# Kernel optimization log

Hardware: AMD Instinct MI355X
Metric: run time of the kernel (lower is better)

The kernel has to match this reference:

```python
import jax, jax.numpy as jnp
import numpy as np

D = 768          # n_embd
I = 3072         # moe_intermediate_size (4 * n_embd)
E = 8            # n_routed_experts
K = 2            # num_experts_per_tok
LIMIT = 10.0     # swiglu_limit
VOCAB = 32768


def setup_inputs() -> dict:
    key = jax.random.key(0)
    ks = jax.random.split(key, 10)
    s = 0.02
    return {
        "x": jax.random.normal(ks[0], (1, 2048, D), dtype=jnp.float32),
        "input_ids": jax.random.randint(ks[1], (1, 2048), 0, VOCAB, dtype=jnp.int64),
        "gate_w": jax.random.normal(ks[2], (D, E), dtype=jnp.float32) * s,
        "gate_bias": jnp.zeros((E,), dtype=jnp.float32),
        "w1": jax.random.normal(ks[3], (E, D, I), dtype=jnp.float32) * s,
        "w2": jax.random.normal(ks[4], (E, I, D), dtype=jnp.float32) * s,
        "w3": jax.random.normal(ks[5], (E, D, I), dtype=jnp.float32) * s,
        "w1s": jax.random.normal(ks[6], (D, I), dtype=jnp.float32) * s,
        "w2s": jax.random.normal(ks[7], (I, D), dtype=jnp.float32) * s,
        "w3s": jax.random.normal(ks[8], (D, I), dtype=jnp.float32) * s,
    }


def _expert(xf, W1, W2, W3):
    # SwiGLU with asymmetric clamping, as in DeepSeekExpert (swiglu_limit > 0)
    gate = jnp.minimum(xf @ W1, LIMIT)               # clamp max only
    up = jnp.clip(xf @ W3, -LIMIT, LIMIT)            # clamp both sides
    return (jax.nn.silu(gate) * up) @ W2


def reference(x, input_ids, gate_w, gate_bias, w1, w2, w3, w1s, w2s, w3s):
    B, T, _ = x.shape
    flat = x.reshape(-1, D)                           # [N, D], N = B*T
    N = flat.shape[0]

    # gating: sqrtsoftplus scoring
    scores = jnp.sqrt(jax.nn.softplus(flat @ gate_w))  # [N, E]
    routed_scores = scores + gate_bias                 # gate_bias used only for topk selection
    _, indices = jax.lax.top_k(routed_scores, K)       # [N, K]

    weights = jnp.take_along_axis(scores, indices, axis=1)  # [N, K]
    # norm_topk_prob=True; routed_scaling_factor=1.0
    weights = weights / jnp.clip(weights.sum(axis=-1, keepdims=True), 1e-6)

    # dense combine matrix [N, E] (jit-friendly dispatch/combine)
    combine = jnp.zeros((N, E), dtype=weights.dtype)
    combine = combine.at[jnp.arange(N)[:, None], indices].add(weights)

    # shared expert on all tokens
    y = _expert(flat, w1s, w2s, w3s)                   # [N, D]

    # routed experts: batched grouped GEMM over all tokens, then weighted combine
    gate_h = jnp.minimum(jnp.einsum('td,edi->eti', flat, w1), LIMIT)   # [E, N, I]
    up_h = jnp.clip(jnp.einsum('td,edi->eti', flat, w3), -LIMIT, LIMIT)
    h = jax.nn.silu(gate_h) * up_h                     # [E, N, I]
    out_e = jnp.einsum('eti,eid->etd', h, w2)          # [E, N, D]
    routed = jnp.einsum('etd,te->td', out_e, combine)  # [N, D]

    return (y + routed).reshape(B, T, D)
```

## Files before the change

kernel.cpp:

```cpp
#include <hip/hip_runtime.h>


#define D_ 768
#define I_ 3072
#define E_ 8
#define NTOK 2048
#define NPMAX 5120
#define MAXTILES 40
#define NSHT 16

typedef __bf16 bf16x8 __attribute__((ext_vector_type(8)));
typedef float floatx4 __attribute__((ext_vector_type(4)));

__device__ __forceinline__ unsigned short f2b(float f) {
    unsigned int u = __float_as_uint(f);
    u += 0x7fffu + ((u >> 16) & 1u);
    return (unsigned short)(u >> 16);
}


__global__ void tcast_kernel(const float* __restrict__ src,
                             unsigned short* __restrict__ dst, int R, int C) {
    __shared__ float t[32][33];
    const float* s = src + (size_t)blockIdx.z * R * C;
    unsigned short* d = dst + (size_t)blockIdx.z * R * C;
    int c0 = blockIdx.x * 32, r0 = blockIdx.y * 32;
    int tx = threadIdx.x & 31, ty = threadIdx.x >> 5;
#pragma unroll
    for (int j = 0; j < 4; j++) {
        int r = ty + j * 8;
        t[r][tx] = s[(size_t)(r0 + r) * C + c0 + tx];
    }
    __syncthreads();
#pragma unroll
    for (int j = 0; j < 4; j++) {
        int c = ty + j * 8;
        d[(size_t)(c0 + c) * R + r0 + tx] = f2b(t[tx][c]);
    }
}

__global__ void cast_x_kernel(const float* __restrict__ x,
                              unsigned short* __restrict__ xb) {
    int gid = blockIdx.x * 256 + threadIdx.x;
    float4 v = *(const float4*)(x + (size_t)gid * 4);
    ushort4 o;
    o.x = f2b(v.x); o.y = f2b(v.y); o.z = f2b(v.z); o.w = f2b(v.w);
    *(ushort4*)(xb + (size_t)gid * 4) = o;
}


__global__ void gate_topk_kernel(const float* __restrict__ x,
                                 const float* __restrict__ gw,
                                 const float* __restrict__ gb,
                                 int* __restrict__ idx, float* __restrict__ wts) {
    int t = blockIdx.x * 4 + (threadIdx.x >> 6);
    int lane = threadIdx.x & 63;
    float z[E_];
#pragma unroll
    for (int e = 0; e < E_; e++) z[e] = 0.f;
    const float* xr = x + (size_t)t * D_;
    for (int j = lane; j < D_; j += 64) {
        float xv = xr[j];
        const float* g = gw + (size_t)j * E_;
#pragma unroll
        for (int e = 0; e < E_; e++) z[e] += xv * g[e];
    }
#pragma unroll
    for (int off = 32; off > 0; off >>= 1)
#pragma unroll
        for (int e = 0; e < E_; e++) z[e] += __shfl_down(z[e], off, 64);
    if (lane == 0) {
        float s[E_], r[E_];
#pragma unroll
        for (int e = 0; e < E_; e++) {
            float zz = z[e];
            float sp = zz > 0.f ? zz + log1pf(expf(-zz)) : log1pf(expf(zz));
            s[e] = sqrtf(sp);
            r[e] = s[e] + gb[e];
        }
        int i0 = 0;
        for (int e = 1; e < E_; e++) if (r[e] > r[i0]) i0 = e;
        int i1 = (i0 == 0) ? 1 : 0;
        for (int e = 0; e < E_; e++) if (e != i0 && r[e] > r[i1]) i1 = e;
        float w0 = s[i0], w1 = s[i1];
        float inv = 1.f / fmaxf(w0 + w1, 1e-6f);
        idx[2 * t] = i0; idx[2 * t + 1] = i1;
        wts[2 * t] = w0 * inv; wts[2 * t + 1] = w1 * inv;
    }
}


__global__ void route_build_kernel(const int* __restrict__ idx,
                                   const float* __restrict__ wts,
                                   int* __restrict__ pair_token,
                                   float* __restrict__ pair_w,
                                   int* __restrict__ pos_of,
                                   int* __restrict__ tiles) {
    __shared__ int cnt[E_], seg[E_], cur[E_];
    int tid = threadIdx.x;
    if (tid < E_) { cnt[tid] = 0; cur[tid] = 0; }
    __syncthreads();
    for (int p = tid; p < NTOK * 2; p += 256) atomicAdd(&cnt[idx[p]], 1);
    __syncthreads();
    if (tid == 0) {
        int off = 0, nt = 0;
        for (int e = 0; e < E_; e++) {
            seg[e] = off;
            int te = (cnt[e] + 127) >> 7;
            for (int j = 0; j < te; j++) {
                tiles[nt * 2] = e; tiles[nt * 2 + 1] = off + j * 128; nt++;
            }
            off += te * 128;
        }
        for (; nt < MAXTILES; nt++) { tiles[nt * 2] = -1; tiles[nt * 2 + 1] = 0; }
    }
    for (int p = tid; p < NPMAX; p += 256) pair_token[p] = -1;
    __syncthreads();
    for (int p = tid; p < NTOK * 2; p += 256) {
        int e = idx[p];
        int r = atomicAdd(&cur[e], 1);
        int pos = seg[e] + r;
        pair_token[pos] = p >> 1;
        pair_w[pos] = wts[p];
        pos_of[p] = pos;
    }
}

__global__ void gather_kernel(const unsigned short* __restrict__ xb,
                              const int* __restrict__ pair_token,
                              unsigned short* __restrict__ xg) {
    int gid = blockIdx.x * 256 + threadIdx.x;
    int p = gid / (D_ / 8);
    int j = (gid % (D_ / 8)) * 8;
    int t = pair_token[p];
    int4 v = make_int4(0, 0, 0, 0);
    if (t >= 0) v = *(const int4*)(xb + (size_t)t * D_ + j);
    *(int4*)(xg + (size_t)p * D_ + j) = v;
}


__launch_bounds__(256)
__global__ void gemm_act_kernel(const unsigned short* __restrict__ xb,
                                const unsigned short* __restrict__ xg,
                                const unsigned short* __restrict__ w1sb,
                                const unsigned short* __restrict__ w3sb,
                                const unsigned short* __restrict__ w1b,
                                const unsigned short* __restrict__ w3b,
                                const int* __restrict__ tiles,
                                unsigned short* __restrict__ act_s,
                                unsigned short* __restrict__ act_r) {
    __shared__ __align__(16) unsigned short As[128 * 40];
    __shared__ __align__(16) unsigned short Bs1[64 * 40];
    __shared__ __align__(16) unsigned short Bs3[64 * 40];

    int mt = blockIdx.y;
    const unsigned short *A, *B1, *B3;
    unsigned short* C;
    int m0;
    if (mt < NSHT) {
        A = xb; B1 = w1sb; B3 = w3sb; C = act_s; m0 = mt * 128;
    } else {
        int e = tiles[(mt - NSHT) * 2];
        if (e < 0) return;
        m0 = tiles[(mt - NSHT) * 2 + 1];
        A = xg; B1 = w1b + (size_t)e * I_ * D_; B3 = w3b + (size_t)e * I_ * D_;
        C = act_r;
    }
    int n0 = blockIdx.x * 64;
    int tid = threadIdx.x;
    int lane = tid & 63, wave = tid >> 6;
    int wm = (wave & 1) * 64, wn = (wave >> 1) * 32;
    int l15 = lane & 15, quad = lane >> 4;

    int arow0 = tid >> 2, cc0 = (tid & 3) * 8;
    int arow1 = arow0 + 64;
    int brow = tid >> 2;

    floatx4 acc1[4][2] = {}; floatx4 acc3[4][2] = {};

    for (int k0 = 0; k0 < D_; k0 += 32) {
        __syncthreads();
        int4 va0 = *(const int4*)(A + (size_t)(m0 + arow0) * D_ + k0 + cc0);
        int4 va1 = *(const int4*)(A + (size_t)(m0 + arow1) * D_ + k0 + cc0);
        int4 vb1 = *(const int4*)(B1 + (size_t)(n0 + brow) * D_ + k0 + cc0);
        int4 vb3 = *(const int4*)(B3 + (size_t)(n0 + brow) * D_ + k0 + cc0);
        *(int4*)(As + arow0 * 40 + cc0) = va0;
        *(int4*)(As + arow1 * 40 + cc0) = va1;
        *(int4*)(Bs1 + brow * 40 + cc0) = vb1;
        *(int4*)(Bs3 + brow * 40 + cc0) = vb3;
        __syncthreads();

        bf16x8 af[4], b1f[2], b3f[2];
#pragma unroll
        for (int mi = 0; mi < 4; mi++)
            af[mi] = *(const bf16x8*)(As + (wm + mi * 16 + l15) * 40 + quad * 8);
#pragma unroll
        for (int ni = 0; ni < 2; ni++) {
            b1f[ni] = *(const bf16x8*)(Bs1 + (wn + ni * 16 + l15) * 40 + quad * 8);
            b3f[ni] = *(const bf16x8*)(Bs3 + (wn + ni * 16 + l15) * 40 + quad * 8);
        }
#pragma unroll
        for (int mi = 0; mi < 4; mi++)
#pragma unroll
            for (int ni = 0; ni < 2; ni++) {
                acc1[mi][ni] = __builtin_amdgcn_mfma_f32_16x16x32_bf16(
                    af[mi], b1f[ni], acc1[mi][ni], 0, 0, 0);
                acc3[mi][ni] = __builtin_amdgcn_mfma_f32_16x16x32_bf16(
                    af[mi], b3f[ni], acc3[mi][ni], 0, 0, 0);
            }
    }

#pragma unroll
    for (int mi = 0; mi < 4; mi++)
#pragma unroll
        for (int ni = 0; ni < 2; ni++) {
            int col = n0 + wn + ni * 16 + l15;
#pragma unroll
            for (int r = 0; r < 4; r++) {
                int row = m0 + wm + mi * 16 + quad * 4 + r;
                float g = fminf(acc1[mi][ni][r], 10.f);
                float u = fminf(fmaxf(acc3[mi][ni][r], -10.f), 10.f);
                float a = g / (1.f + __expf(-g)) * u;
                C[(size_t)row * I_ + col] = f2b(a);
            }
        }
}


__launch_bounds__(256)
__global__ void gemm_out_kernel(const unsigned short* __restrict__ act_s,
                                const unsigned short* __restrict__ act_r,
                                const unsigned short* __restrict__ w2sb,
                                const unsigned short* __restrict__ w2b,
                                const int* __restrict__ tiles,
                                float* __restrict__ y_s, float* __restrict__ ro) {
    __shared__ __align__(16) unsigned short As[128 * 40];
    __shared__ __align__(16) unsigned short Bs[64 * 40];

    int mt = blockIdx.y;
    const unsigned short *A, *B;
    float* C;
    int m0;
    if (mt < NSHT) {
        A = act_s; B = w2sb; C = y_s; m0 = mt * 128;
    } else {
        int e = tiles[(mt - NSHT) * 2];
        if (e < 0) return;
        m0 = tiles[(mt - NSHT) * 2 + 1];
        A = act_r; B = w2b + (size_t)e * I_ * D_; C = ro;
    }
    int n0 = blockIdx.x * 64;
    int tid = threadIdx.x;
    int lane = tid & 63, wave = tid >> 6;
    int wm = (wave & 1) * 64, wn = (wave >> 1) * 32;
    int l15 = lane & 15, quad = lane >> 4;

    int arow0 = tid >> 2, cc0 = (tid & 3) * 8;
    int arow1 = arow0 + 64;
    int brow = tid >> 2;

    floatx4 acc[4][2] = {};

    for (int k0 = 0; k0 < I_; k0 += 32) {
        __syncthreads();
        int4 va0 = *(const int4*)(A + (size_t)(m0 + arow0) * I_ + k0 + cc0);
        int4 va1 = *(const int4*)(A + (size_t)(m0 + arow1) * I_ + k0 + cc0);
        int4 vb  = *(const int4*)(B + (size_t)(n0 + brow) * I_ + k0 + cc0);
        *(int4*)(As + arow0 * 40 + cc0) = va0;
        *(int4*)(As + arow1 * 40 + cc0) = va1;
        *(int4*)(Bs + brow * 40 + cc0) = vb;
        __syncthreads();

        bf16x8 af[4], bf[2];
#pragma unroll
        for (int mi = 0; mi < 4; mi++)
            af[mi] = *(const bf16x8*)(As + (wm + mi * 16 + l15) * 40 + quad * 8);
#pragma unroll
        for (int ni = 0; ni < 2; ni++)
            bf[ni] = *(const bf16x8*)(Bs + (wn + ni * 16 + l15) * 40 + quad * 8);
#pragma unroll
        for (int mi = 0; mi < 4; mi++)
#pragma unroll
            for (int ni = 0; ni < 2; ni++)
                acc[mi][ni] = __builtin_amdgcn_mfma_f32_16x16x32_bf16(
                    af[mi], bf[ni], acc[mi][ni], 0, 0, 0);
    }

#pragma unroll
    for (int mi = 0; mi < 4; mi++)
#pragma unroll
        for (int ni = 0; ni < 2; ni++) {
            int col = n0 + wn + ni * 16 + l15;
#pragma unroll
            for (int r = 0; r < 4; r++) {
                int row = m0 + wm + mi * 16 + quad * 4 + r;
                C[(size_t)row * D_ + col] = acc[mi][ni][r];
            }
        }
}


__global__ void combine_kernel(const float* __restrict__ y_s,
                               const float* __restrict__ ro,
                               const int* __restrict__ pos_of,
                               const float* __restrict__ pair_w,
                               float* __restrict__ out) {
    int gid = blockIdx.x * 256 + threadIdx.x;
    int t = gid / (D_ / 4);
    int j = (gid % (D_ / 4)) * 4;
    int p0 = pos_of[2 * t], p1 = pos_of[2 * t + 1];
    float w0 = pair_w[p0], w1 = pair_w[p1];
    float4 a = *(const float4*)(y_s + (size_t)t * D_ + j);
    float4 b = *(const float4*)(ro + (size_t)p0 * D_ + j);
    float4 c = *(const float4*)(ro + (size_t)p1 * D_ + j);
    float4 o;
    o.x = a.x + w0 * b.x + w1 * c.x;
    o.y = a.y + w0 * b.y + w1 * c.y;
    o.z = a.z + w0 * b.z + w1 * c.z;
    o.w = a.w + w0 * b.w + w1 * c.w;
    *(float4*)(out + (size_t)t * D_ + j) = o;
}


extern "C" void kernel_launch(void* const* d_in, const int* in_sizes, int n_in,
                              void* d_out, int out_size, void* d_ws, size_t ws_size,
                              hipStream_t stream) {
    (void)in_sizes; (void)n_in; (void)out_size; (void)ws_size;
    const float* x   = (const float*)d_in[0];
    const float* gw  = (const float*)d_in[2];
    const float* gb  = (const float*)d_in[3];
    const float* w1  = (const float*)d_in[4];
    const float* w2  = (const float*)d_in[5];
    const float* w3  = (const float*)d_in[6];
    const float* w1s = (const float*)d_in[7];
    const float* w2s = (const float*)d_in[8];
    const float* w3s = (const float*)d_in[9];
    float* out = (float*)d_out;

    char* ws = (char*)d_ws;
    size_t off = 0;
    auto alloc = [&](size_t bytes) {
        size_t o = (off + 255) & ~(size_t)255;
        off = o + bytes;
        return (void*)(ws + o);
    };
    unsigned short* xb   = (unsigned short*)alloc((size_t)NTOK * D_ * 2);
    unsigned short* xg   = (unsigned short*)alloc((size_t)NPMAX * D_ * 2);
    unsigned short* w1b  = (unsigned short*)alloc((size_t)E_ * I_ * D_ * 2);
    unsigned short* w3b  = (unsigned short*)alloc((size_t)E_ * I_ * D_ * 2);
    unsigned short* w2b  = (unsigned short*)alloc((size_t)E_ * I_ * D_ * 2);
    unsigned short* w1sb = (unsigned short*)alloc((size_t)I_ * D_ * 2);
    unsigned short* w3sb = (unsigned short*)alloc((size_t)I_ * D_ * 2);
    unsigned short* w2sb = (unsigned short*)alloc((size_t)I_ * D_ * 2);
    unsigned short* acts = (unsigned short*)alloc((size_t)NTOK * I_ * 2);
    unsigned short* actr = (unsigned short*)alloc((size_t)NPMAX * I_ * 2);
    float* ys   = (float*)alloc((size_t)NTOK * D_ * 4);
    float* rout = (float*)alloc((size_t)NPMAX * D_ * 4);
    int*   idx  = (int*)alloc((size_t)NTOK * 2 * 4);
    float* wts  = (float*)alloc((size_t)NTOK * 2 * 4);
    int*   ptok = (int*)alloc((size_t)NPMAX * 4);
    float* pw   = (float*)alloc((size_t)NPMAX * 4);
    int*   posf = (int*)alloc((size_t)NTOK * 2 * 4);
    int*   tls  = (int*)alloc((size_t)MAXTILES * 2 * 4);

    tcast_kernel<<<dim3(I_ / 32, D_ / 32, E_), 256, 0, stream>>>(w1, w1b, D_, I_);
    tcast_kernel<<<dim3(I_ / 32, D_ / 32, E_), 256, 0, stream>>>(w3, w3b, D_, I_);
    tcast_kernel<<<dim3(D_ / 32, I_ / 32, E_), 256, 0, stream>>>(w2, w2b, I_, D_);
    tcast_kernel<<<dim3(I_ / 32, D_ / 32, 1), 256, 0, stream>>>(w1s, w1sb, D_, I_);
    tcast_kernel<<<dim3(I_ / 32, D_ / 32, 1), 256, 0, stream>>>(w3s, w3sb, D_, I_);
    tcast_kernel<<<dim3(D_ / 32, I_ / 32, 1), 256, 0, stream>>>(w2s, w2sb, I_, D_);

    cast_x_kernel<<<NTOK * D_ / 4 / 256, 256, 0, stream>>>(x, xb);
    gate_topk_kernel<<<NTOK / 4, 256, 0, stream>>>(x, gw, gb, idx, wts);
    route_build_kernel<<<1, 256, 0, stream>>>(idx, wts, ptok, pw, posf, tls);
    gather_kernel<<<NPMAX * (D_ / 8) / 256, 256, 0, stream>>>(xb, ptok, xg);

    gemm_act_kernel<<<dim3(I_ / 64, NSHT + MAXTILES), 256, 0, stream>>>(
        xb, xg, w1sb, w3sb, w1b, w3b, tls, acts, actr);
    gemm_out_kernel<<<dim3(D_ / 64, NSHT + MAXTILES), 256, 0, stream>>>(
        acts, actr, w2sb, w2b, tls, ys, rout);
    combine_kernel<<<NTOK * (D_ / 4) / 256, 256, 0, stream>>>(ys, rout, posf, pw, out);
}
```

Baseline: 519.4 us.

## Use direct global-to-LDS loads in GEMMs and fuse wider weight transpose-cast kernels

Replaces the register-staged global→LDS tile copies in both GEMM kernels with global_load_lds 16-byte direct loads, dropping the LDS row padding (stride 40→32) so each wave writes a contiguous 16-row slab. The six weight transpose/cast launches become two launches with 64x64 tiles, float4 reads and 16-byte bf16 writes. The aim is fewer VGPR round-trips and instructions on the load path and less launch overhead and narrower memory traffic in the weight casting. Removing the padding may introduce LDS bank conflicts on the fragment reads.

Result: faster. 474.1 us (-8.7%).

```diff
diff --git a/kernel.cpp b/kernel.cpp
--- a/kernel.cpp
+++ b/kernel.cpp
@@ -12,6 +12,10 @@
 typedef __bf16 bf16x8 __attribute__((ext_vector_type(8)));
 typedef float floatx4 __attribute__((ext_vector_type(4)));
 
+#define GLOAD_LDS16(g, l) __builtin_amdgcn_global_load_lds( \
+    (const __attribute__((address_space(1))) void*)(g),     \
+    (__attribute__((address_space(3))) void*)(l), 16, 0, 0)
+
 __device__ __forceinline__ unsigned short f2b(float f) {
     unsigned int u = __float_as_uint(f);
     u += 0x7fffu + ((u >> 16) & 1u);
@@ -19,24 +23,61 @@
 }
 
 
-__global__ void tcast_kernel(const float* __restrict__ src,
-                             unsigned short* __restrict__ dst, int R, int C) {
-    __shared__ float t[32][33];
-    const float* s = src + (size_t)blockIdx.z * R * C;
-    unsigned short* d = dst + (size_t)blockIdx.z * R * C;
-    int c0 = blockIdx.x * 32, r0 = blockIdx.y * 32;
-    int tx = threadIdx.x & 31, ty = threadIdx.x >> 5;
+template <int R, int C>
+__device__ __forceinline__ void tbody(const float* __restrict__ s,
+                                      unsigned short* __restrict__ d) {
+    __shared__ float t[64][65];
+    int c0 = blockIdx.x * 64, r0 = blockIdx.y * 64;
+    int tid = threadIdx.x;
 #pragma unroll
     for (int j = 0; j < 4; j++) {
-        int r = ty + j * 8;
-        t[r][tx] = s[(size_t)(r0 + r) * C + c0 + tx];
+        int slot = tid + j * 256;
+        int r = slot >> 4;
+        int c4 = (slot & 15) * 4;
+        float4 v = *(const float4*)(s + (size_t)(r0 + r) * C + c0 + c4);
+        t[r][c4] = v.x; t[r][c4 + 1] = v.y; t[r][c4 + 2] = v.z; t[r][c4 + 3] = v.w;
     }
     __syncthreads();
 #pragma unroll
-    for (int j = 0; j < 4; j++) {
-        int c = ty + j * 8;
-        d[(size_t)(c0 + c) * R + r0 + tx] = f2b(t[tx][c]);
-    }
+    for (int j = 0; j < 2; j++) {
+        int slot = tid + j * 256;
+        int c = slot >> 3;
+        int rs = (slot & 7) * 8;
+        unsigned short o[8];
+#pragma unroll
+        for (int i = 0; i < 8; i++) o[i] = f2b(t[rs + i][c]);
+        *(int4*)(d + (size_t)(c0 + c) * R + r0 + rs) = *(const int4*)o;
+    }
+}
+
+__global__ void tcastDI_kernel(const float* __restrict__ w1,
+                               const float* __restrict__ w3,
+                               const float* __restrict__ w1s,
+                               const float* __restrict__ w3s,
+                               unsigned short* __restrict__ w1b,
+                               unsigned short* __restrict__ w3b,
+                               unsigned short* __restrict__ w1sb,
+                               unsigned short* __restrict__ w3sb) {
+    int z = blockIdx.z;
+    const float* s;
+    unsigned short* d;
+    if (z < 8)        { s = w1 + (size_t)z * D_ * I_;       d = w1b + (size_t)z * D_ * I_; }
+    else if (z < 16)  { s = w3 + (size_t)(z - 8) * D_ * I_; d = w3b + (size_t)(z - 8) * D_ * I_; }
+    else if (z == 16) { s = w1s; d = w1sb; }
+    else              { s = w3s; d = w3sb; }
+    tbody<D_, I_>(s, d);
+}
+
+__global__ void tcastID_kernel(const float* __restrict__ w2,
+                               const float* __restrict__ w2s,
+                               unsigned short* __restrict__ w2b,
+                               unsigned short* __restrict__ w2sb) {
+    int z = blockIdx.z;
+    const float* s;
+    unsigned short* d;
+    if (z < 8) { s = w2 + (size_t)z * I_ * D_; d = w2b + (size_t)z * I_ * D_; }
+    else       { s = w2s; d = w2sb; }
+    tbody<I_, D_>(s, d);
 }
 
 __global__ void cast_x_kernel(const float* __restrict__ x,
@@ -149,9 +190,9 @@
                                 const int* __restrict__ tiles,
                                 unsigned short* __restrict__ act_s,
                                 unsigned short* __restrict__ act_r) {
-    __shared__ __align__(16) unsigned short As[128 * 40];
-    __shared__ __align__(16) unsigned short Bs1[64 * 40];
-    __shared__ __align__(16) unsigned short Bs3[64 * 40];
+    __shared__ __align__(16) unsigned short As[128 * 32];
+    __shared__ __align__(16) unsigned short Bs1[64 * 32];
+    __shared__ __align__(16) unsigned short Bs3[64 * 32];
 
     int mt = blockIdx.y;
     const unsigned short *A, *B1, *B3;
@@ -171,33 +212,35 @@
     int lane = tid & 63, wave = tid >> 6;
     int wm = (wave & 1) * 64, wn = (wave >> 1) * 32;
     int l15 = lane & 15, quad = lane >> 4;
-
-    int arow0 = tid >> 2, cc0 = (tid & 3) * 8;
-    int arow1 = arow0 + 64;
-    int brow = tid >> 2;
+    int l4 = lane >> 2, c8 = (lane & 3) * 8;
+
+    const unsigned short* Ap0 = A + (size_t)(m0 + wave * 16 + l4) * D_ + c8;
+    const unsigned short* Ap1 = Ap0 + (size_t)64 * D_;
+    const unsigned short* B1p = B1 + (size_t)(n0 + wave * 16 + l4) * D_ + c8;
+    const unsigned short* B3p = B3 + (size_t)(n0 + wave * 16 + l4) * D_ + c8;
+    unsigned short* AsW0 = As + wave * 16 * 32;
+    unsigned short* AsW1 = As + (64 + wave * 16) * 32;
+    unsigned short* Bs1W = Bs1 + wave * 16 * 32;
+    unsigned short* Bs3W = Bs3 + wave * 16 * 32;
 
     floatx4 acc1[4][2] = {}; floatx4 acc3[4][2] = {};
 
     for (int k0 = 0; k0 < D_; k0 += 32) {
         __syncthreads();
-        int4 va0 = *(const int4*)(A + (size_t)(m0 + arow0) * D_ + k0 + cc0);
-        int4 va1 = *(const int4*)(A + (size_t)(m0 + arow1) * D_ + k0 + cc0);
-        int4 vb1 = *(const int4*)(B1 + (size_t)(n0 + brow) * D_ + k0 + cc0);
-        int4 vb3 = *(const int4*)(B3 + (size_t)(n0 + brow) * D_ + k0 + cc0);
-        *(int4*)(As + arow0 * 40 + cc0) = va0;
-        *(int4*)(As + arow1 * 40 + cc0) = va1;
-        *(int4*)(Bs1 + brow * 40 + cc0) = vb1;
-        *(int4*)(Bs3 + brow * 40 + cc0) = vb3;
+        GLOAD_LDS16(Ap0 + k0, AsW0);
+        GLOAD_LDS16(Ap1 + k0, AsW1);
+        GLOAD_LDS16(B1p + k0, Bs1W);
+        GLOAD_LDS16(B3p + k0, Bs3W);
         __syncthreads();
 
         bf16x8 af[4], b1f[2], b3f[2];
 #pragma unroll
         for (int mi = 0; mi < 4; mi++)
-            af[mi] = *(const bf16x8*)(As + (wm + mi * 16 + l15) * 40 + quad * 8);
+            af[mi] = *(const bf16x8*)(As + (wm + mi * 16 + l15) * 32 + quad * 8);
 #pragma unroll
         for (int ni = 0; ni < 2; ni++) {
-            b1f[ni] = *(const bf16x8*)(Bs1 + (wn + ni * 16 + l15) * 40 + quad * 8);
-            b3f[ni] = *(const bf16x8*)(Bs3 + (wn + ni * 16 + l15) * 40 + quad * 8);
+            b1f[ni] = *(const bf16x8*)(Bs1 + (wn + ni * 16 + l15) * 32 + quad * 8);
+            b3f[ni] = *(const bf16x8*)(Bs3 + (wn + ni * 16 + l15) * 32 + quad * 8);
         }
 #pragma unroll
         for (int mi = 0; mi < 4; mi++)
@@ -234,8 +277,8 @@
                                 const unsigned short* __restrict__ w2b,
                                 const int* __restrict__ tiles,
                                 float* __restrict__ y_s, float* __restrict__ ro) {
-    __shared__ __align__(16) unsigned short As[128 * 40];
-    __shared__ __align__(16) unsigned short Bs[64 * 40];
+    __shared__ __align__(16) unsigned short As[128 * 32];
+    __shared__ __align__(16) unsigned short Bs[64 * 32];
 
     int mt = blockIdx.y;
     const unsigned short *A, *B;
@@ -254,30 +297,31 @@
     int lane = tid & 63, wave = tid >> 6;
     int wm = (wave & 1) * 64, wn = (wave >> 1) * 32;
     int l15 = lane & 15, quad = lane >> 4;
-
-    int arow0 = tid >> 2, cc0 = (tid & 3) * 8;
-    int arow1 = arow0 + 64;
-    int brow = tid >> 2;
+    int l4 = lane >> 2, c8 = (lane & 3) * 8;
+
+    const unsigned short* Ap0 = A + (size_t)(m0 + wave * 16 + l4) * I_ + c8;
+    const unsigned short* Ap1 = Ap0 + (size_t)64 * I_;
+    const unsigned short* Bp  = B + (size_t)(n0 + wave * 16 + l4) * I_ + c8;
+    unsigned short* AsW0 = As + wave * 16 * 32;
+    unsigned short* AsW1 = As + (64 + wave * 16) * 32;
+    unsigned short* BsW  = Bs + wave * 16 * 32;
 
     floatx4 acc[4][2] = {};
 
     for (int k0 = 0; k0 < I_; k0 += 32) {
         __syncthreads();
-        int4 va0 = *(const int4*)(A + (size_t)(m0 + arow0) * I_ + k0 + cc0);
-        int4 va1 = *(const int4*)(A + (size_t)(m0 + arow1) * I_ + k0 + cc0);
-        int4 vb  = *(const int4*)(B + (size_t)(n0 + brow) * I_ + k0 + cc0);
-        *(int4*)(As + arow0 * 40 + cc0) = va0;
-        *(int4*)(As + arow1 * 40 + cc0) = va1;
-        *(int4*)(Bs + brow * 40 + cc0) = vb;
+        GLOAD_LDS16(Ap0 + k0, AsW0);
+        GLOAD_LDS16(Ap1 + k0, AsW1);
+        GLOAD_LDS16(Bp + k0, BsW);
         __syncthreads();
 
         bf16x8 af[4], bf[2];
 #pragma unroll
         for (int mi = 0; mi < 4; mi++)
-            af[mi] = *(const bf16x8*)(As + (wm + mi * 16 + l15) * 40 + quad * 8);
+            af[mi] = *(const bf16x8*)(As + (wm + mi * 16 + l15) * 32 + quad * 8);
 #pragma unroll
         for (int ni = 0; ni < 2; ni++)
-            bf[ni] = *(const bf16x8*)(Bs + (wn + ni * 16 + l15) * 40 + quad * 8);
+            bf[ni] = *(const bf16x8*)(Bs + (wn + ni * 16 + l15) * 32 + quad * 8);
 #pragma unroll
         for (int mi = 0; mi < 4; mi++)
 #pragma unroll
@@ -363,12 +407,10 @@
     int*   posf = (int*)alloc((size_t)NTOK * 2 * 4);
     int*   tls  = (int*)alloc((size_t)MAXTILES * 2 * 4);
 
-    tcast_kernel<<<dim3(I_ / 32, D_ / 32, E_), 256, 0, stream>>>(w1, w1b, D_, I_);
-    tcast_kernel<<<dim3(I_ / 32, D_ / 32, E_), 256, 0, stream>>>(w3, w3b, D_, I_);
-    tcast_kernel<<<dim3(D_ / 32, I_ / 32, E_), 256, 0, stream>>>(w2, w2b, I_, D_);
-    tcast_kernel<<<dim3(I_ / 32, D_ / 32, 1), 256, 0, stream>>>(w1s, w1sb, D_, I_);
-    tcast_kernel<<<dim3(I_ / 32, D_ / 32, 1), 256, 0, stream>>>(w3s, w3sb, D_, I_);
-    tcast_kernel<<<dim3(D_ / 32, I_ / 32, 1), 256, 0, stream>>>(w2s, w2sb, I_, D_);
+    tcastDI_kernel<<<dim3(I_ / 64, D_ / 64, 18), 256, 0, stream>>>(
+        w1, w3, w1s, w3s, w1b, w3b, w1sb, w3sb);
+    tcastID_kernel<<<dim3(D_ / 64, I_ / 64, 9), 256, 0, stream>>>(
+        w2, w2s, w2b, w2sb);
 
     cast_x_kernel<<<NTOK * D_ / 4 / 256, 256, 0, stream>>>(x, xb);
     gate_topk_kernel<<<NTOK / 4, 256, 0, stream>>>(x, gw, gb, idx, wts);
```
